# Optimization experiments

Measured on AMD Instinct MI355X. Metric: run time of the kernel, lower is better.

Reference implementation:

```python
import jax, jax.numpy as jnp
import numpy as np

TEMPERATURE = 0.1

def setup_inputs() -> dict:
    key = jax.random.key(0)
    k1, k2 = jax.random.split(key)
    B, D = 8192, 512
    anchor = jax.random.normal(k1, (B, D), dtype=jnp.float32)
    positive = jax.random.normal(k2, (B, D), dtype=jnp.float32)
    return {"anchor": anchor, "positive": positive}

def reference(anchor, positive):
    # sim[i, j] = <anchor_i, positive_j> / T  -- [B, B]
    sim = jnp.einsum("bd,nd->bn", anchor, positive) / TEMPERATURE
    # InfoNCE with in-batch negatives: positive is the diagonal; since softmax
    # is permutation-invariant, -log_softmax(logits)[pos] = logsumexp(row) - diag.
    loss = jax.nn.logsumexp(sim, axis=1) - jnp.diagonal(sim)
    return jnp.mean(loss)
```

## Files before the change

kernel.cpp:

```cpp
#include <hip/hip_runtime.h>
#include <hip/hip_bf16.h>
#include <math.h>
#include <stdint.h>


#define NB 8192
#define DDIM 512
#define SPLITS 16
#define BM 128
#define BN 128
#define CPB (NB / SPLITS)
#define NROUND 32

#define DELTA 0.045f
#define INV_DELTA (1.0f / DELTA)
#define OUT_SCALE (DELTA * DELTA * 10.0f)
#define K2F (OUT_SCALE * 1.4426950408889634f)
#define LN2F 0.6931471805599453f

typedef unsigned char u8;
typedef __attribute__((ext_vector_type(4))) int i32x4;

__device__ __forceinline__ float fexp2(float x) {
#if __has_builtin(__builtin_amdgcn_exp2f)
  return __builtin_amdgcn_exp2f(x);
#else
  return __expf(x * LN2F);
#endif
}
__device__ __forceinline__ float flog2(float x) {
#if __has_builtin(__builtin_amdgcn_logf)
  return __builtin_amdgcn_logf(x);
#else
  return __logf(x) * 1.4426950408889634f;
#endif
}

__device__ __forceinline__ void gl2lds16(const u8* g, const u8* l) {
  __builtin_amdgcn_global_load_lds(
      (__attribute__((address_space(1))) unsigned int*)(uintptr_t)g,
      (__attribute__((address_space(3))) unsigned int*)(unsigned int)(uintptr_t)l,
      16, 0, 0);
}

__device__ __forceinline__ unsigned pack4(float x0, float x1, float x2, float x3) {
  int q0 = min(127, max(-127, __float2int_rn(x0 * INV_DELTA)));
  int q1 = min(127, max(-127, __float2int_rn(x1 * INV_DELTA)));
  int q2 = min(127, max(-127, __float2int_rn(x2 * INV_DELTA)));
  int q3 = min(127, max(-127, __float2int_rn(x3 * INV_DELTA)));
  return (q0 & 0xFF) | ((q1 & 0xFF) << 8) | ((q2 & 0xFF) << 16) | ((q3 & 0xFF) << 24);
}

__global__ void cvt_diag_kernel(const float* __restrict__ a, const float* __restrict__ p,
                                u8* __restrict__ aq, u8* __restrict__ pq,
                                float* __restrict__ diag, float* __restrict__ out) {
  if (blockIdx.x == 0 && threadIdx.x == 0) out[0] = 0.f;
  int row = (blockIdx.x * 256 + threadIdx.x) >> 6;
  int lane = threadIdx.x & 63;
  const float4* ar = (const float4*)(a + (size_t)row * DDIM + lane * 8);
  const float4* pr = (const float4*)(p + (size_t)row * DDIM + lane * 8);
  float4 a0 = ar[0], a1 = ar[1];
  float4 p0 = pr[0], p1 = pr[1];
  *(uint2*)(aq + (size_t)row * DDIM + lane * 8) =
      (uint2){pack4(a0.x, a0.y, a0.z, a0.w), pack4(a1.x, a1.y, a1.z, a1.w)};
  *(uint2*)(pq + (size_t)row * DDIM + lane * 8) =
      (uint2){pack4(p0.x, p0.y, p0.z, p0.w), pack4(p1.x, p1.y, p1.z, p1.w)};
  float s = a0.x * p0.x + a0.y * p0.y + a0.z * p0.z + a0.w * p0.w +
            a1.x * p1.x + a1.y * p1.y + a1.z * p1.z + a1.w * p1.w;
  for (int off = 32; off > 0; off >>= 1) s += __shfl_down(s, off);
  if (lane == 0) diag[row] = s * 10.0f;
}

__global__ __launch_bounds__(256, 4) void gemm_lse(
    const u8* __restrict__ Aq, const u8* __restrict__ Bq,
    float* __restrict__ partLse) {
  __shared__ u8 sA[2][BM * 64];
  __shared__ u8 sB[2][BN * 64];
  __shared__ float sMm[2][BM];
  __shared__ float sMl[2][BM];

  const int tid = threadIdx.x;
  const int wave = tid >> 6;
  const int lane = tid & 63;
  const int quad = lane >> 4;
  const int l16 = lane & 15;
  const int wr = wave >> 1, wc = wave & 1;

  const int bid = blockIdx.x;
  const int xcd = bid & 7;
  const int idx = bid >> 3;
  const int rowTile = (idx & 7) * 8 + xcd;
  const int colSplit = idx >> 3;
  const int row0 = rowTile * BM;
  const int col0 = colSplit * CPB;

  const int rsub = lane >> 2;
  const int qsrc = (lane & 3) ^ ((rsub >> 1) & 3);
  const u8* aCol = Aq + (size_t)(row0 + wave * 32 + rsub) * DDIM + qsrc * 16;
  const u8* bCol = Bq + (size_t)(col0 + wave * 16 + rsub) * DDIM + qsrc * 16;
  const int ldsOffA = wave * 2048;
  const int ldsOffB = wave * 1024;

  const int sw = (l16 >> 1) & 3;
  const int fragA = (wr * 64 + l16) * 64 + ((quad ^ sw) * 16);
  const int fragB = (wc * 64 + l16) * 64 + ((quad ^ sw) * 16);

#define STAGE(r)                                                        \
  do {                                                                  \
    int _t = (r) >> 3, _kk = ((r) & 7) << 6, _bf = (r) & 1;             \
    const u8* _a = aCol + _kk;                                          \
    const u8* _b = bCol + _t * (BN * DDIM) + _kk;                       \
    gl2lds16(_a, &sA[_bf][ldsOffA]);                                    \
    gl2lds16(_a + 16 * DDIM, &sA[_bf][ldsOffA + 1024]);                 \
    gl2lds16(_b, &sB[_bf][ldsOffB]);                                    \
    gl2lds16(_b + 64 * DDIM, &sB[_bf][ldsOffB + 4096]);                 \
  } while (0)

  STAGE(0);

  i32x4 acc[4][4];
#pragma unroll
  for (int mi = 0; mi < 4; ++mi)
#pragma unroll
    for (int ni = 0; ni < 4; ++ni) acc[mi][ni] = (i32x4){0, 0, 0, 0};

  float rm[4][4], rl[4][4];
#pragma unroll
  for (int mi = 0; mi < 4; ++mi)
#pragma unroll
    for (int rr = 0; rr < 4; ++rr) { rm[mi][rr] = -INFINITY; rl[mi][rr] = 0.f; }

  for (int r = 0; r < NROUND; ++r) {
    const int buf = r & 1;
    __syncthreads();
    if (r < NROUND - 1) STAGE(r + 1);

    i32x4 bq[4];
#pragma unroll
    for (int ni = 0; ni < 4; ++ni)
      bq[ni] = *(const i32x4*)(&sB[buf][fragB + ni * 16 * 64]);
#pragma unroll
    for (int mi = 0; mi < 4; ++mi) {
      i32x4 af = *(const i32x4*)(&sA[buf][fragA + mi * 16 * 64]);
#pragma unroll
      for (int ni = 0; ni < 4; ++ni)
        acc[mi][ni] = __builtin_amdgcn_mfma_i32_16x16x64_i8(af, bq[ni], acc[mi][ni], 0, 0, 0);
    }

    if ((r & 7) == 7) {
#pragma unroll
      for (int mi = 0; mi < 4; ++mi) {
#pragma unroll
        for (int rr = 0; rr < 4; ++rr) {
          const int i0 = acc[mi][0][rr], i1 = acc[mi][1][rr];
          const int i2 = acc[mi][2][rr], i3 = acc[mi][3][rr];
          const int im = max(max(i0, i1), max(i2, i3));
          const float mf = (float)im * K2F;
          const float nm = fmaxf(rm[mi][rr], mf);
          rl[mi][rr] = rl[mi][rr] * fexp2(rm[mi][rr] - nm) +
                       (fexp2(fmaf((float)i0, K2F, -nm)) +
                        fexp2(fmaf((float)i1, K2F, -nm)) +
                        fexp2(fmaf((float)i2, K2F, -nm)) +
                        fexp2(fmaf((float)i3, K2F, -nm)));
          rm[mi][rr] = nm;
#pragma unroll
          for (int ni = 0; ni < 4; ++ni) acc[mi][ni][rr] = 0;
        }
      }
    }
  }

#pragma unroll
  for (int mi = 0; mi < 4; ++mi) {
#pragma unroll
    for (int rr = 0; rr < 4; ++rr) {
      float m = rm[mi][rr], l = rl[mi][rr];
#pragma unroll
      for (int mask = 1; mask < 16; mask <<= 1) {
        float om = __shfl_xor(m, mask);
        float ol = __shfl_xor(l, mask);
        float nm = fmaxf(m, om);
        l = l * fexp2(m - nm) + ol * fexp2(om - nm);
        m = nm;
      }
      if (l16 == 0) {
        int rowl = wr * 64 + mi * 16 + quad * 4 + rr;
        sMm[wc][rowl] = m;
        sMl[wc][rowl] = l;
      }
    }
  }
  __syncthreads();
  if (tid < BM) {
    float m0 = sMm[0][tid], m1 = sMm[1][tid];
    float l0 = sMl[0][tid], l1 = sMl[1][tid];
    float nm = fmaxf(m0, m1);
    float L = l0 * fexp2(m0 - nm) + l1 * fexp2(m1 - nm);
    partLse[(size_t)colSplit * NB + row0 + tid] = nm + flog2(L);
  }
#undef STAGE
}

__global__ void reduce_kernel(const float* __restrict__ partLse,
                              const float* __restrict__ diag, float* __restrict__ out) {
  __shared__ float red[4];
  int r = blockIdx.x * 256 + threadIdx.x;
  float M = -INFINITY;
#pragma unroll
  for (int s = 0; s < SPLITS; ++s) M = fmaxf(M, partLse[(size_t)s * NB + r]);
  float L = 0.f;
#pragma unroll
  for (int s = 0; s < SPLITS; ++s) L += fexp2(partLse[(size_t)s * NB + r] - M);
  float v = (M + flog2(L)) * LN2F - diag[r];
  for (int off = 32; off > 0; off >>= 1) v += __shfl_down(v, off);
  if ((threadIdx.x & 63) == 0) red[threadIdx.x >> 6] = v;
  __syncthreads();
  if (threadIdx.x == 0) {
    float s = (red[0] + red[1] + red[2] + red[3]) * (1.0f / (float)NB);
    atomicAdd(out, s);
  }
}

extern "C" void kernel_launch(void* const* d_in, const int* in_sizes, int n_in,
                              void* d_out, int out_size, void* d_ws, size_t ws_size,
                              hipStream_t stream) {
  const float* anchor = (const float*)d_in[0];
  const float* positive = (const float*)d_in[1];
  float* out = (float*)d_out;

  char* ws = (char*)d_ws;
  u8* Aq = (u8*)ws;
  u8* Bq = (u8*)(ws + (size_t)4194304);
  float* diag = (float*)(ws + (size_t)8388608);
  float* partLse = (float*)(ws + (size_t)8388608 + 32768);

  cvt_diag_kernel<<<NB / 4, 256, 0, stream>>>(anchor, positive, Aq, Bq, diag, out);
  gemm_lse<<<SPLITS * (NB / BM), 256, 0, stream>>>(Aq, Bq, partLse);
  reduce_kernel<<<NB / 256, 256, 0, stream>>>(partLse, diag, out);
}
```

Before: 129.6 us.

## Enlarge GEMM tiles to 256x256 with 8 waves and 4-stage LDS pipeline

Doubles the block tile to 256x256 with 512 threads and halves the column splits, so each block reuses loaded A/B fragments across more MFMAs. The LDS double buffer becomes a four-stage ring with explicit vmcnt waits and barriers that interleave A/B loads between MFMA halves, plus s_setprio around MFMA bursts. The intent is to raise arithmetic intensity and hide global-to-LDS latency. In exchange it uses more registers (acc 4x8 per wave) and 128KB of LDS, which limits occupancy, and launches only 256 blocks.

```diff
diff --git a/kernel.cpp b/kernel.cpp
--- a/kernel.cpp
+++ b/kernel.cpp
@@ -6,9 +6,9 @@
 
 #define NB 8192
 #define DDIM 512
-#define SPLITS 16
-#define BM 128
-#define BN 128
+#define SPLITS 8
+#define BM 256
+#define BN 256
 #define CPB (NB / SPLITS)
 #define NROUND 32
 
@@ -71,105 +71,156 @@
   if (lane == 0) diag[row] = s * 10.0f;
 }
 
-__global__ __launch_bounds__(256, 4) void gemm_lse(
+__device__ __forceinline__ void fold_lse(i32x4 (&acc)[4][8], float (&rm)[4][4],
+                                         float (&rl)[4][4]) {
+#pragma unroll
+  for (int mi = 0; mi < 4; ++mi) {
+#pragma unroll
+    for (int rr = 0; rr < 4; ++rr) {
+      int im = acc[mi][0][rr];
+#pragma unroll
+      for (int ni = 1; ni < 8; ++ni) im = max(im, acc[mi][ni][rr]);
+      const float mf = (float)im * K2F;
+      const float nm = fmaxf(rm[mi][rr], mf);
+      float add = 0.f;
+#pragma unroll
+      for (int ni = 0; ni < 8; ++ni)
+        add += fexp2(fmaf((float)acc[mi][ni][rr], K2F, -nm));
+      rl[mi][rr] = rl[mi][rr] * fexp2(rm[mi][rr] - nm) + add;
+      rm[mi][rr] = nm;
+#pragma unroll
+      for (int ni = 0; ni < 8; ++ni) acc[mi][ni][rr] = 0;
+    }
+  }
+}
+
+__global__ __launch_bounds__(512, 2) void gemm_lse(
     const u8* __restrict__ Aq, const u8* __restrict__ Bq,
     float* __restrict__ partLse) {
-  __shared__ u8 sA[2][BM * 64];
-  __shared__ u8 sB[2][BN * 64];
-  __shared__ float sMm[2][BM];
-  __shared__ float sMl[2][BM];
+  __shared__ u8 sA[4][BM * 64];
+  __shared__ u8 sB[4][BN * 64];
 
   const int tid = threadIdx.x;
   const int wave = tid >> 6;
   const int lane = tid & 63;
   const int quad = lane >> 4;
   const int l16 = lane & 15;
-  const int wr = wave >> 1, wc = wave & 1;
+  const int wr = wave >> 1;
+  const int wc = wave & 1;
 
   const int bid = blockIdx.x;
   const int xcd = bid & 7;
   const int idx = bid >> 3;
-  const int rowTile = (idx & 7) * 8 + xcd;
-  const int colSplit = idx >> 3;
+  const int rowTile = (idx & 3) * 8 + xcd;
+  const int colSplit = idx >> 2;
   const int row0 = rowTile * BM;
   const int col0 = colSplit * CPB;
 
   const int rsub = lane >> 2;
   const int qsrc = (lane & 3) ^ ((rsub >> 1) & 3);
   const u8* aCol = Aq + (size_t)(row0 + wave * 32 + rsub) * DDIM + qsrc * 16;
-  const u8* bCol = Bq + (size_t)(col0 + wave * 16 + rsub) * DDIM + qsrc * 16;
-  const int ldsOffA = wave * 2048;
-  const int ldsOffB = wave * 1024;
+  const u8* bCol = Bq + (size_t)(col0 + wave * 32 + rsub) * DDIM + qsrc * 16;
+  const int ldsOff = wave * 2048;
 
   const int sw = (l16 >> 1) & 3;
   const int fragA = (wr * 64 + l16) * 64 + ((quad ^ sw) * 16);
-  const int fragB = (wc * 64 + l16) * 64 + ((quad ^ sw) * 16);
-
-#define STAGE(r)                                                        \
-  do {                                                                  \
-    int _t = (r) >> 3, _kk = ((r) & 7) << 6, _bf = (r) & 1;             \
-    const u8* _a = aCol + _kk;                                          \
-    const u8* _b = bCol + _t * (BN * DDIM) + _kk;                       \
-    gl2lds16(_a, &sA[_bf][ldsOffA]);                                    \
-    gl2lds16(_a + 16 * DDIM, &sA[_bf][ldsOffA + 1024]);                 \
-    gl2lds16(_b, &sB[_bf][ldsOffB]);                                    \
-    gl2lds16(_b + 64 * DDIM, &sB[_bf][ldsOffB + 4096]);                 \
+  const int fragB = (wc * 128 + l16) * 64 + ((quad ^ sw) * 16);
+
+  i32x4 acc[4][8];
+#pragma unroll
+  for (int mi = 0; mi < 4; ++mi)
+#pragma unroll
+    for (int ni = 0; ni < 8; ++ni) acc[mi][ni] = (i32x4){0, 0, 0, 0};
+
+  float rm[4][4], rl[4][4];
+#pragma unroll
+  for (int mi = 0; mi < 4; ++mi)
+#pragma unroll
+    for (int rr = 0; rr < 4; ++rr) { rm[mi][rr] = -INFINITY; rl[mi][rr] = 0.f; }
+
+#define STAGE_A(t)                                                       \
+  do {                                                                   \
+    const int _kk = ((t) & 7) << 6, _bf = (t) & 3;                       \
+    const u8* _a = aCol + _kk;                                           \
+    gl2lds16(_a, &sA[_bf][ldsOff]);                                      \
+    gl2lds16(_a + 16 * DDIM, &sA[_bf][ldsOff + 1024]);                   \
   } while (0)
-
-  STAGE(0);
-
-  i32x4 acc[4][4];
-#pragma unroll
-  for (int mi = 0; mi < 4; ++mi)
-#pragma unroll
-    for (int ni = 0; ni < 4; ++ni) acc[mi][ni] = (i32x4){0, 0, 0, 0};
-
-  float rm[4][4], rl[4][4];
-#pragma unroll
-  for (int mi = 0; mi < 4; ++mi)
-#pragma unroll
-    for (int rr = 0; rr < 4; ++rr) { rm[mi][rr] = -INFINITY; rl[mi][rr] = 0.f; }
-
-  for (int r = 0; r < NROUND; ++r) {
-    const int buf = r & 1;
-    __syncthreads();
-    if (r < NROUND - 1) STAGE(r + 1);
-
-    i32x4 bq[4];
-#pragma unroll
-    for (int ni = 0; ni < 4; ++ni)
-      bq[ni] = *(const i32x4*)(&sB[buf][fragB + ni * 16 * 64]);
-#pragma unroll
-    for (int mi = 0; mi < 4; ++mi) {
-      i32x4 af = *(const i32x4*)(&sA[buf][fragA + mi * 16 * 64]);
-#pragma unroll
-      for (int ni = 0; ni < 4; ++ni)
-        acc[mi][ni] = __builtin_amdgcn_mfma_i32_16x16x64_i8(af, bq[ni], acc[mi][ni], 0, 0, 0);
-    }
-
-    if ((r & 7) == 7) {
-#pragma unroll
-      for (int mi = 0; mi < 4; ++mi) {
-#pragma unroll
-        for (int rr = 0; rr < 4; ++rr) {
-          const int i0 = acc[mi][0][rr], i1 = acc[mi][1][rr];
-          const int i2 = acc[mi][2][rr], i3 = acc[mi][3][rr];
-          const int im = max(max(i0, i1), max(i2, i3));
-          const float mf = (float)im * K2F;
-          const float nm = fmaxf(rm[mi][rr], mf);
-          rl[mi][rr] = rl[mi][rr] * fexp2(rm[mi][rr] - nm) +
-                       (fexp2(fmaf((float)i0, K2F, -nm)) +
-                        fexp2(fmaf((float)i1, K2F, -nm)) +
-                        fexp2(fmaf((float)i2, K2F, -nm)) +
-                        fexp2(fmaf((float)i3, K2F, -nm)));
-          rm[mi][rr] = nm;
-#pragma unroll
-          for (int ni = 0; ni < 4; ++ni) acc[mi][ni][rr] = 0;
-        }
-      }
-    }
-  }
-
+#define STAGE_B(t)                                                       \
+  do {                                                                   \
+    const int _kk = ((t) & 7) << 6, _bf = (t) & 3;                       \
+    const u8* _b = bCol + ((t) >> 3) * (BN * DDIM) + _kk;                \
+    gl2lds16(_b, &sB[_bf][ldsOff]);                                      \
+    gl2lds16(_b + 16 * DDIM, &sB[_bf][ldsOff + 1024]);                   \
+  } while (0)
+
+  STAGE_A(0); STAGE_B(0);
+  STAGE_A(1); STAGE_B(1);
+  STAGE_A(2); STAGE_B(2);
+  asm volatile("s_waitcnt vmcnt(8)");
+  __builtin_amdgcn_s_barrier();
+
+#define MF8(AR, MI)                                                                 \
+  acc[MI][0] = __builtin_amdgcn_mfma_i32_16x16x64_i8(AR, bq0, acc[MI][0], 0, 0, 0); \
+  acc[MI][1] = __builtin_amdgcn_mfma_i32_16x16x64_i8(AR, bq1, acc[MI][1], 0, 0, 0); \
+  acc[MI][2] = __builtin_amdgcn_mfma_i32_16x16x64_i8(AR, bq2, acc[MI][2], 0, 0, 0); \
+  acc[MI][3] = __builtin_amdgcn_mfma_i32_16x16x64_i8(AR, bq3, acc[MI][3], 0, 0, 0); \
+  acc[MI][4] = __builtin_amdgcn_mfma_i32_16x16x64_i8(AR, bq4, acc[MI][4], 0, 0, 0); \
+  acc[MI][5] = __builtin_amdgcn_mfma_i32_16x16x64_i8(AR, bq5, acc[MI][5], 0, 0, 0); \
+  acc[MI][6] = __builtin_amdgcn_mfma_i32_16x16x64_i8(AR, bq6, acc[MI][6], 0, 0, 0); \
+  acc[MI][7] = __builtin_amdgcn_mfma_i32_16x16x64_i8(AR, bq7, acc[MI][7], 0, 0, 0);
+
+#define TILE_BODY(r, DO_STAGE)                                           \
+  do {                                                                   \
+    const int _b = (r) & 3;                                              \
+    const u8* _sa = &sA[_b][0];                                          \
+    const u8* _sb = &sB[_b][0];                                          \
+    i32x4 bq0 = *(const i32x4*)(_sb + fragB + 0 * 1024);                 \
+    i32x4 bq1 = *(const i32x4*)(_sb + fragB + 1 * 1024);                 \
+    i32x4 bq2 = *(const i32x4*)(_sb + fragB + 2 * 1024);                 \
+    i32x4 bq3 = *(const i32x4*)(_sb + fragB + 3 * 1024);                 \
+    i32x4 bq4 = *(const i32x4*)(_sb + fragB + 4 * 1024);                 \
+    i32x4 bq5 = *(const i32x4*)(_sb + fragB + 5 * 1024);                 \
+    i32x4 bq6 = *(const i32x4*)(_sb + fragB + 6 * 1024);                 \
+    i32x4 bq7 = *(const i32x4*)(_sb + fragB + 7 * 1024);                 \
+    i32x4 a0 = *(const i32x4*)(_sa + fragA + 0 * 1024);                  \
+    i32x4 a1 = *(const i32x4*)(_sa + fragA + 1 * 1024);                  \
+    if (DO_STAGE) STAGE_A((r) + 3);                                      \
+    __builtin_amdgcn_s_barrier();                                        \
+    asm volatile("s_waitcnt lgkmcnt(0)");                                \
+    __builtin_amdgcn_s_setprio(1);                                       \
+    MF8(a0, 0) MF8(a1, 1)                                                \
+    __builtin_amdgcn_s_setprio(0);                                       \
+    __builtin_amdgcn_s_barrier();                                        \
+    i32x4 a2 = *(const i32x4*)(_sa + fragA + 2 * 1024);                  \
+    i32x4 a3 = *(const i32x4*)(_sa + fragA + 3 * 1024);                  \
+    if (DO_STAGE) STAGE_B((r) + 3);                                      \
+    __builtin_amdgcn_s_barrier();                                        \
+    asm volatile("s_waitcnt lgkmcnt(0)");                                \
+    __builtin_amdgcn_s_setprio(1);                                       \
+    MF8(a2, 2) MF8(a3, 3)                                                \
+    __builtin_amdgcn_s_setprio(0);                                       \
+    if (((r) & 7) == 7) fold_lse(acc, rm, rl);                           \
+  } while (0)
+
+  for (int r = 0; r < NROUND - 3; ++r) {
+    TILE_BODY(r, 1);
+    asm volatile("s_waitcnt vmcnt(8)");
+    __builtin_amdgcn_s_barrier();
+  }
+  TILE_BODY(NROUND - 3, 0);
+  asm volatile("s_waitcnt vmcnt(4)");
+  __builtin_amdgcn_s_barrier();
+  TILE_BODY(NROUND - 2, 0);
+  asm volatile("s_waitcnt vmcnt(0)");
+  __builtin_amdgcn_s_barrier();
+  TILE_BODY(NROUND - 1, 0);
+  __builtin_amdgcn_s_barrier();
+#undef TILE_BODY
+#undef MF8
+#undef STAGE_A
+#undef STAGE_B
+
+  float2* const scr = (float2*)&sA[0][0];
 #pragma unroll
   for (int mi = 0; mi < 4; ++mi) {
 #pragma unroll
@@ -185,20 +236,17 @@
       }
       if (l16 == 0) {
         int rowl = wr * 64 + mi * 16 + quad * 4 + rr;
-        sMm[wc][rowl] = m;
-        sMl[wc][rowl] = l;
+        scr[wc * 256 + rowl] = (float2){m, l};
       }
     }
   }
   __syncthreads();
   if (tid < BM) {
-    float m0 = sMm[0][tid], m1 = sMm[1][tid];
-    float l0 = sMl[0][tid], l1 = sMl[1][tid];
-    float nm = fmaxf(m0, m1);
-    float L = l0 * fexp2(m0 - nm) + l1 * fexp2(m1 - nm);
+    float2 p0 = scr[tid], p1 = scr[256 + tid];
+    float nm = fmaxf(p0.x, p1.x);
+    float L = p0.y * fexp2(p0.x - nm) + p1.y * fexp2(p1.x - nm);
     partLse[(size_t)colSplit * NB + row0 + tid] = nm + flog2(L);
   }
-#undef STAGE
 }
 
 __global__ void reduce_kernel(const float* __restrict__ partLse,
@@ -235,6 +283,6 @@
   float* partLse = (float*)(ws + (size_t)8388608 + 32768);
 
   cvt_diag_kernel<<<NB / 4, 256, 0, stream>>>(anchor, positive, Aq, Bq, diag, out);
-  gemm_lse<<<SPLITS * (NB / BM), 256, 0, stream>>>(Aq, Bq, partLse);
+  gemm_lse<<<SPLITS * (NB / BM), 512, 0, stream>>>(Aq, Bq, partLse);
   reduce_kernel<<<NB / 256, 256, 0, stream>>>(partLse, diag, out);
 }
```

Result: faster. 120.7 us (-6.9%).

## Triple-buffer LDS staging with prefetch distance two and one barrier per round

Applied to the files above, without the earlier changes.

Moves the GEMM main loop from a double-buffered LDS pipeline to a triple-buffered one. Loads for round r+2 are issued after the fragments for the current round are read, and each round ends with a partial vmcnt wait and a single barrier, so global-to-LDS copies can overlap more of the MFMA work. The B-tile staging layout changes to match A (32 rows per wave at stride 16*DDIM). Occupancy drops from 4 to 3 blocks per CU because of the larger LDS footprint, and the hand-written waitcnt counts must stay correct for the async LDS loads.

```diff
diff --git a/kernel.cpp b/kernel.cpp
--- a/kernel.cpp
+++ b/kernel.cpp
@@ -71,11 +71,34 @@
   if (lane == 0) diag[row] = s * 10.0f;
 }
 
-__global__ __launch_bounds__(256, 4) void gemm_lse(
+__device__ __forceinline__ void fold_lse(i32x4 (&acc)[4][4], float (&rm)[4][4],
+                                         float (&rl)[4][4]) {
+#pragma unroll
+  for (int mi = 0; mi < 4; ++mi) {
+#pragma unroll
+    for (int rr = 0; rr < 4; ++rr) {
+      const int i0 = acc[mi][0][rr], i1 = acc[mi][1][rr];
+      const int i2 = acc[mi][2][rr], i3 = acc[mi][3][rr];
+      const int im = max(max(i0, i1), max(i2, i3));
+      const float mf = (float)im * K2F;
+      const float nm = fmaxf(rm[mi][rr], mf);
+      rl[mi][rr] = rl[mi][rr] * fexp2(rm[mi][rr] - nm) +
+                   (fexp2(fmaf((float)i0, K2F, -nm)) +
+                    fexp2(fmaf((float)i1, K2F, -nm)) +
+                    fexp2(fmaf((float)i2, K2F, -nm)) +
+                    fexp2(fmaf((float)i3, K2F, -nm)));
+      rm[mi][rr] = nm;
+#pragma unroll
+      for (int ni = 0; ni < 4; ++ni) acc[mi][ni][rr] = 0;
+    }
+  }
+}
+
+__global__ __launch_bounds__(256, 3) void gemm_lse(
     const u8* __restrict__ Aq, const u8* __restrict__ Bq,
     float* __restrict__ partLse) {
-  __shared__ u8 sA[2][BM * 64];
-  __shared__ u8 sB[2][BN * 64];
+  __shared__ u8 sA[3][BM * 64];
+  __shared__ u8 sB[3][BN * 64];
   __shared__ float sMm[2][BM];
   __shared__ float sMl[2][BM];
 
@@ -97,78 +120,82 @@
   const int rsub = lane >> 2;
   const int qsrc = (lane & 3) ^ ((rsub >> 1) & 3);
   const u8* aCol = Aq + (size_t)(row0 + wave * 32 + rsub) * DDIM + qsrc * 16;
-  const u8* bCol = Bq + (size_t)(col0 + wave * 16 + rsub) * DDIM + qsrc * 16;
-  const int ldsOffA = wave * 2048;
-  const int ldsOffB = wave * 1024;
+  const u8* bCol = Bq + (size_t)(col0 + wave * 32 + rsub) * DDIM + qsrc * 16;
+  const int ldsOff = wave * 2048;
 
   const int sw = (l16 >> 1) & 3;
   const int fragA = (wr * 64 + l16) * 64 + ((quad ^ sw) * 16);
   const int fragB = (wc * 64 + l16) * 64 + ((quad ^ sw) * 16);
 
-#define STAGE(r)                                                        \
-  do {                                                                  \
-    int _t = (r) >> 3, _kk = ((r) & 7) << 6, _bf = (r) & 1;             \
-    const u8* _a = aCol + _kk;                                          \
-    const u8* _b = bCol + _t * (BN * DDIM) + _kk;                       \
-    gl2lds16(_a, &sA[_bf][ldsOffA]);                                    \
-    gl2lds16(_a + 16 * DDIM, &sA[_bf][ldsOffA + 1024]);                 \
-    gl2lds16(_b, &sB[_bf][ldsOffB]);                                    \
-    gl2lds16(_b + 64 * DDIM, &sB[_bf][ldsOffB + 4096]);                 \
+  i32x4 acc[4][4];
+#pragma unroll
+  for (int mi = 0; mi < 4; ++mi)
+#pragma unroll
+    for (int ni = 0; ni < 4; ++ni) acc[mi][ni] = (i32x4){0, 0, 0, 0};
+
+  float rm[4][4], rl[4][4];
+#pragma unroll
+  for (int mi = 0; mi < 4; ++mi)
+#pragma unroll
+    for (int rr = 0; rr < 4; ++rr) { rm[mi][rr] = -INFINITY; rl[mi][rr] = 0.f; }
+
+#define STAGE(t, BOFF)                                                   \
+  do {                                                                   \
+    const int _kk = ((t) & 7) << 6;                                      \
+    const u8* _a = aCol + _kk;                                           \
+    const u8* _b = bCol + ((t) >> 3) * (BN * DDIM) + _kk;                \
+    gl2lds16(_a, &sA[0][(BOFF) + ldsOff]);                               \
+    gl2lds16(_a + 16 * DDIM, &sA[0][(BOFF) + ldsOff + 1024]);            \
+    gl2lds16(_b, &sB[0][(BOFF) + ldsOff]);                               \
+    gl2lds16(_b + 16 * DDIM, &sB[0][(BOFF) + ldsOff + 1024]);            \
   } while (0)
 
-  STAGE(0);
-
-  i32x4 acc[4][4];
-#pragma unroll
-  for (int mi = 0; mi < 4; ++mi)
-#pragma unroll
-    for (int ni = 0; ni < 4; ++ni) acc[mi][ni] = (i32x4){0, 0, 0, 0};
-
-  float rm[4][4], rl[4][4];
-#pragma unroll
-  for (int mi = 0; mi < 4; ++mi)
-#pragma unroll
-    for (int rr = 0; rr < 4; ++rr) { rm[mi][rr] = -INFINITY; rl[mi][rr] = 0.f; }
-
-  for (int r = 0; r < NROUND; ++r) {
-    const int buf = r & 1;
-    __syncthreads();
-    if (r < NROUND - 1) STAGE(r + 1);
-
-    i32x4 bq[4];
-#pragma unroll
-    for (int ni = 0; ni < 4; ++ni)
-      bq[ni] = *(const i32x4*)(&sB[buf][fragB + ni * 16 * 64]);
-#pragma unroll
-    for (int mi = 0; mi < 4; ++mi) {
-      i32x4 af = *(const i32x4*)(&sA[buf][fragA + mi * 16 * 64]);
-#pragma unroll
-      for (int ni = 0; ni < 4; ++ni)
-        acc[mi][ni] = __builtin_amdgcn_mfma_i32_16x16x64_i8(af, bq[ni], acc[mi][ni], 0, 0, 0);
+  STAGE(0, 0);
+  STAGE(1, 8192);
+  asm volatile("s_waitcnt vmcnt(4)");
+  __builtin_amdgcn_s_barrier();
+
+#define MF4(AR, MI)                                                                 \
+  acc[MI][0] = __builtin_amdgcn_mfma_i32_16x16x64_i8(AR, bq0, acc[MI][0], 0, 0, 0); \
+  acc[MI][1] = __builtin_amdgcn_mfma_i32_16x16x64_i8(AR, bq1, acc[MI][1], 0, 0, 0); \
+  acc[MI][2] = __builtin_amdgcn_mfma_i32_16x16x64_i8(AR, bq2, acc[MI][2], 0, 0, 0); \
+  acc[MI][3] = __builtin_amdgcn_mfma_i32_16x16x64_i8(AR, bq3, acc[MI][3], 0, 0, 0);
+
+#define ROUND_BODY(BF, DO_STAGE, T2, SBF)                                \
+  do {                                                                   \
+    const u8* _sa = &sA[0][0] + (BF) * 8192;                             \
+    const u8* _sb = &sB[0][0] + (BF) * 8192;                             \
+    i32x4 bq0 = *(const i32x4*)(_sb + fragB + 0 * 1024);                 \
+    i32x4 bq1 = *(const i32x4*)(_sb + fragB + 1 * 1024);                 \
+    i32x4 bq2 = *(const i32x4*)(_sb + fragB + 2 * 1024);                 \
+    i32x4 bq3 = *(const i32x4*)(_sb + fragB + 3 * 1024);                 \
+    i32x4 a0 = *(const i32x4*)(_sa + fragA + 0 * 1024);                  \
+    i32x4 a1 = *(const i32x4*)(_sa + fragA + 1 * 1024);                  \
+    i32x4 a2 = *(const i32x4*)(_sa + fragA + 2 * 1024);                  \
+    i32x4 a3 = *(const i32x4*)(_sa + fragA + 3 * 1024);                  \
+    if (DO_STAGE) STAGE(T2, (SBF) * 8192);                               \
+    MF4(a0, 0) MF4(a1, 1) MF4(a2, 2) MF4(a3, 3)                          \
+  } while (0)
+
+  {
+    int bf = 0, sbf = 2;
+    for (int r = 0; r < NROUND - 2; ++r) {
+      ROUND_BODY(bf, 1, r + 2, sbf);
+      if ((r & 7) == 7) fold_lse(acc, rm, rl);
+      asm volatile("s_waitcnt vmcnt(4)");
+      __builtin_amdgcn_s_barrier();
+      bf = (bf == 2) ? 0 : bf + 1;
+      sbf = (sbf == 2) ? 0 : sbf + 1;
     }
-
-    if ((r & 7) == 7) {
-#pragma unroll
-      for (int mi = 0; mi < 4; ++mi) {
-#pragma unroll
-        for (int rr = 0; rr < 4; ++rr) {
-          const int i0 = acc[mi][0][rr], i1 = acc[mi][1][rr];
-          const int i2 = acc[mi][2][rr], i3 = acc[mi][3][rr];
-          const int im = max(max(i0, i1), max(i2, i3));
-          const float mf = (float)im * K2F;
-          const float nm = fmaxf(rm[mi][rr], mf);
-          rl[mi][rr] = rl[mi][rr] * fexp2(rm[mi][rr] - nm) +
-                       (fexp2(fmaf((float)i0, K2F, -nm)) +
-                        fexp2(fmaf((float)i1, K2F, -nm)) +
-                        fexp2(fmaf((float)i2, K2F, -nm)) +
-                        fexp2(fmaf((float)i3, K2F, -nm)));
-          rm[mi][rr] = nm;
-#pragma unroll
-          for (int ni = 0; ni < 4; ++ni) acc[mi][ni][rr] = 0;
-        }
-      }
-    }
-  }
+  }
+  ROUND_BODY(0, 0, 0, 0);
+  asm volatile("s_waitcnt vmcnt(0)");
+  __builtin_amdgcn_s_barrier();
+  ROUND_BODY(1, 0, 0, 0);
+  fold_lse(acc, rm, rl);
+#undef ROUND_BODY
+#undef MF4
+#undef STAGE
 
 #pragma unroll
   for (int mi = 0; mi < 4; ++mi) {
@@ -198,7 +225,6 @@
     float L = l0 * fexp2(m0 - nm) + l1 * fexp2(m1 - nm);
     partLse[(size_t)colSplit * NB + row0 + tid] = nm + flog2(L);
   }
-#undef STAGE
 }
 
 __global__ void reduce_kernel(const float* __restrict__ partLse,
```

After: 125.7 us. -3.0%, faster.
